# Kernel optimization log

Hardware: AMD Instinct MI355X
Metric: run time of the kernel (lower is better)

## Reference

```python
import jax, jax.numpy as jnp
import numpy as np
import math

B, S, D, H, FF, NB = 32, 512, 512, 8, 2048, 2
DK = D // H  # 64
NEG = -1e30  # stands in for torch's -1e32 (fp32-safe)


def _make_pe():
    # CosinePositionalEmbedding: deterministic sin/cos part (the 0.1*randn is fully overwritten)
    pos = np.arange(S, dtype=np.float32)[:, None]
    div = np.exp(np.arange(0, D, 2, dtype=np.float32) * -(math.log(10000.0) / D))
    pe = np.zeros((S, D), np.float32)
    pe[:, 0::2] = np.sin(pos * div)
    pe[:, 1::2] = np.cos(pos * div)
    return jnp.asarray(pe)[None]  # [1, S, D]


def setup_inputs() -> dict:
    key = jax.random.key(0)
    ks = jax.random.split(key, 10)
    def w(k, shape):
        return jax.random.normal(k, shape, jnp.float32) * 0.02
    return {
        "q_embed_data": jax.random.normal(ks[0], (B, S, D), jnp.float32),
        "qa_embed_data": jax.random.normal(ks[1], (B, S, D), jnp.float32),
        "forget_rate": jax.random.uniform(ks[2], (B, 1, S, 1), jnp.float32),
        "pe": _make_pe(),
        "Wk": w(ks[3], (NB, D, D)), "bk": jnp.zeros((NB, D), jnp.float32),
        "Wv": w(ks[4], (NB, D, D)), "bv": jnp.zeros((NB, D), jnp.float32),
        "Wo": w(ks[5], (NB, D, D)), "bo": jnp.zeros((NB, D), jnp.float32),
        "g1": jnp.ones((NB, D), jnp.float32), "be1": jnp.zeros((NB, D), jnp.float32),
        "W1": w(ks[6], (NB, D, FF)), "bf1": jnp.zeros((NB, FF), jnp.float32),
        "W2": w(ks[7], (NB, FF, D)), "bf2": jnp.zeros((NB, D), jnp.float32),
        "g2": jnp.ones((NB, D), jnp.float32), "be2": jnp.zeros((NB, D), jnp.float32),
    }


def _ln(x, g, b):
    m = jnp.mean(x, axis=-1, keepdims=True)
    v = jnp.var(x, axis=-1, keepdims=True)
    return (x - m) * jax.lax.rsqrt(v + 1e-5) * g + b


def reference(q_embed_data, qa_embed_data, forget_rate, pe, Wk, bk, Wv, bv, Wo, bo,
              g1, be1, W1, bf1, W2, bf2, g2, be2):
    x = q_embed_data + pe[:, :S]   # query stream
    y = qa_embed_data + pe[:, :S]  # value stream (constant across blocks)
    # mask==0 path: src_mask True where triu(k=0)==0, i.e. strictly-past positions j < i
    allowed = jnp.tril(jnp.ones((S, S), bool), k=-1)
    scale = 1.0 / math.sqrt(DK)
    for i in range(NB):
        # kq_same=True: q and k both use k_linear; query=key=x so q == k
        q = (x @ Wk[i] + bk[i]).reshape(B, S, H, DK).transpose(0, 2, 1, 3)  # [B,H,S,dk]
        k = q
        v = (y @ Wv[i] + bv[i]).reshape(B, S, H, DK).transpose(0, 2, 1, 3)
        scores = jnp.einsum('bhqd,bhkd->bhqk', q, k) * scale      # [B,H,S,S]
        scores = scores * forget_rate                              # broadcast [B,1,S,1]
        scores = jnp.where(allowed, scores, NEG)                   # masked_fill(mask==0, -1e32)
        attn = jax.nn.softmax(scores, axis=-1)
        attn = attn.at[:, :, 0, :].set(0.0)                        # zero_pad first query row
        out = jnp.einsum('bhqk,bhkd->bhqd', attn, v)
        out = out.transpose(0, 2, 1, 3).reshape(B, S, D) @ Wo[i] + bo[i]
        x = _ln(x + out, g1[i], be1[i])
        ffn = jax.nn.relu(x @ W1[i] + bf1[i]) @ W2[i] + bf2[i]
        x = _ln(x + ffn, g2[i], be2[i])
    return x
```

## Files before the change

### kernel.cpp

```cpp
#include <hip/hip_runtime.h>

#define B_ 32
#define S_ 512
#define D_ 512
#define H_ 8
#define DK_ 64
#define FF_ 2048

typedef float f32x4 __attribute__((ext_vector_type(4)));
typedef __bf16 bf16x8 __attribute__((ext_vector_type(8)));
typedef __bf16 bf16x4 __attribute__((ext_vector_type(4)));

__device__ __forceinline__ void gld_lds16(const void* gptr, void* lptr) {
    auto g = (__attribute__((address_space(1))) void*)(unsigned long long)gptr;
    auto l = (__attribute__((address_space(3))) void*)(unsigned)(unsigned long long)lptr;
    __builtin_amdgcn_global_load_lds(g, l, 16, 0, 0);
}

__global__ __launch_bounds__(256) void prep_kernel(
    const float* __restrict__ q, const float* __restrict__ qa,
    const float* __restrict__ pe, __bf16* __restrict__ xbf,
    __bf16* __restrict__ ybf)
{
    const int n4 = B_ * S_ * D_ / 4;
    for (int i = blockIdx.x * blockDim.x + threadIdx.x; i < n4;
         i += gridDim.x * blockDim.x) {
        float4 pv = ((const float4*)pe)[i & (S_ * D_ / 4 - 1)];
        float4 qv = ((const float4*)q)[i];
        float4 av = ((const float4*)qa)[i];
        bf16x4 xb = {(__bf16)(qv.x + pv.x), (__bf16)(qv.y + pv.y),
                     (__bf16)(qv.z + pv.z), (__bf16)(qv.w + pv.w)};
        ((bf16x4*)xbf)[i] = xb;
        bf16x4 yb = {(__bf16)(av.x + pv.x), (__bf16)(av.y + pv.y),
                     (__bf16)(av.z + pv.z), (__bf16)(av.w + pv.w)};
        ((bf16x4*)ybf)[i] = yb;
    }
}

__device__ __forceinline__ void ttile(
    const float* __restrict__ in, __bf16* __restrict__ out,
    int R, int C, int bx, int by, int t)
{
    __shared__ float tile[32][33];
    const int tc = bx * 32, tr = by * 32;
    const int lx = t & 31, ly = t >> 5;
    #pragma unroll
    for (int yy = ly; yy < 32; yy += 8)
        tile[yy][lx] = in[(long)(tr + yy) * C + tc + lx];
    __syncthreads();
    #pragma unroll
    for (int yy = ly; yy < 32; yy += 8)
        out[(long)(tc + yy) * R + tr + lx] = (__bf16)tile[lx][yy];
}

__global__ __launch_bounds__(256) void transpose_all(
    const float* __restrict__ Wk, const float* __restrict__ Wv,
    const float* __restrict__ Wo, const float* __restrict__ W1,
    const float* __restrict__ W2, __bf16* __restrict__ ok,
    __bf16* __restrict__ ov, __bf16* __restrict__ oo,
    __bf16* __restrict__ o1, __bf16* __restrict__ o2)
{
    const int id = blockIdx.x, t = threadIdx.x;
    if (id < 1536) {
        const int z = id >> 8, r = id & 255;
        const int sel = z >> 1, i = z & 1;
        const float* src = sel == 0 ? Wk : (sel == 1 ? Wv : Wo);
        __bf16* dst = sel == 0 ? ok : (sel == 1 ? ov : oo);
        ttile(src + (long)i * 262144, dst + (long)i * 262144, 512, 512,
              r & 15, r >> 4, t);
    } else if (id < 3584) {
        int r = id - 1536; const int i = r >> 10; r &= 1023;
        ttile(W1 + (long)i * 1048576, o1 + (long)i * 1048576, 512, 2048,
              r & 63, r >> 6, t);
    } else {
        int r = id - 3584; const int i = r >> 10; r &= 1023;
        ttile(W2 + (long)i * 1048576, o2 + (long)i * 1048576, 2048, 512,
              r & 15, r >> 4, t);
    }
}

template <int RELU, int MODE>
__global__ __launch_bounds__(256) void gemm_kernel(
    const __bf16* __restrict__ A, const __bf16* __restrict__ Bt,
    const float* __restrict__ bias, const __bf16* __restrict__ res,
    __bf16* __restrict__ out, int M, int N, int K)
{
    __shared__ __bf16 As[2][128 * 64];
    __shared__ __bf16 Bs[2][128 * 64];
    const int t = threadIdx.x;
    const int lane = t & 63;
    const int wv = t >> 6, wr = wv >> 1, wc = wv & 1;
    const int lr = lane & 15, lk = lane >> 4;

    const int nwg = gridDim.x * gridDim.y;
    const int lin = blockIdx.y * gridDim.x + blockIdx.x;
    const int swz = (lin & 7) * (nwg >> 3) + (lin >> 3);
    const int m0 = (swz / gridDim.x) * 128, n0 = (swz % gridDim.x) * 128;

    const int srow = t >> 3;
    const int sslot = (t & 7) ^ (srow & 7);
    const __bf16* gA = A + (long)(m0 + srow) * K + sslot * 8;
    const __bf16* gB = Bt + (long)(n0 + srow) * K + sslot * 8;
    const long rstep = (long)32 * K;

    auto STAGE = [&](int bsel, int k0) {
        char* ldsA = (char*)As[bsel] + t * 16;
        char* ldsB = (char*)Bs[bsel] + t * 16;
        #pragma unroll
        for (int u = 0; u < 4; ++u) {
            gld_lds16(gA + u * rstep + k0, ldsA + u * 4096);
            gld_lds16(gB + u * rstep + k0, ldsB + u * 4096);
        }
    };

    f32x4 acc[4][4] = {};
    auto COMPUTE = [&](int bsel) {
        #pragma unroll
        for (int kk = 0; kk < 2; ++kk) {
            bf16x8 af[4], bfr[4];
            #pragma unroll
            for (int i = 0; i < 4; ++i) {
                const int rr = wr * 64 + i * 16 + lr;
                af[i] = *(const bf16x8*)((const char*)As[bsel] +
                        (rr << 7) + (((kk * 4 + lk) ^ (rr & 7)) << 4));
            }
            #pragma unroll
            for (int j = 0; j < 4; ++j) {
                const int rr = wc * 64 + j * 16 + lr;
                bfr[j] = *(const bf16x8*)((const char*)Bs[bsel] +
                         (rr << 7) + (((kk * 4 + lk) ^ (rr & 7)) << 4));
            }
            #pragma unroll
            for (int i = 0; i < 4; ++i)
                #pragma unroll
                for (int j = 0; j < 4; ++j)
                    acc[i][j] = __builtin_amdgcn_mfma_f32_16x16x32_bf16(
                        af[i], bfr[j], acc[i][j], 0, 0, 0);
        }
    };

    const int NT = K >> 6;
    STAGE(0, 0);
    STAGE(1, 64);
    for (int kt = 0; kt < NT - 1; ++kt) {
        asm volatile("s_waitcnt vmcnt(8)" ::: "memory");
        __builtin_amdgcn_s_barrier();
        COMPUTE(kt & 1);
        __builtin_amdgcn_s_barrier();
        if (kt + 2 < NT) STAGE(kt & 1, (kt + 2) << 6);
    }
    asm volatile("s_waitcnt vmcnt(0)" ::: "memory");
    __builtin_amdgcn_s_barrier();
    COMPUTE((NT - 1) & 1);

    #pragma unroll
    for (int i = 0; i < 4; ++i) {
        #pragma unroll
        for (int j = 0; j < 4; ++j) {
            const int n = n0 + wc * 64 + j * 16 + lr;
            const float bv = bias[n];
            #pragma unroll
            for (int r = 0; r < 4; ++r) {
                const int m = m0 + wr * 64 + i * 16 + lk * 4 + r;
                const long off = (long)m * N + n;
                float v = acc[i][j][r] + bv;
                if (MODE == 1) v += (float)res[off];
                if (RELU) v = v > 0.f ? v : 0.f;
                out[off] = (__bf16)v;
            }
        }
    }
}

__global__ __launch_bounds__(256) void gemm_kv(
    const __bf16* __restrict__ xbf, const __bf16* __restrict__ ybf,
    const __bf16* __restrict__ wkt, const __bf16* __restrict__ wvt,
    const float* __restrict__ bk, const float* __restrict__ bv,
    __bf16* __restrict__ kout, __bf16* __restrict__ vtout)
{
    constexpr int N = 512, K = 512;
    __shared__ __bf16 As[2][128 * 64];
    __shared__ __bf16 Bs[2][128 * 64];
    const int t = threadIdx.x;
    const int lane = t & 63;
    const int wv = t >> 6, wr = wv >> 1, wc = wv & 1;
    const int lr = lane & 15, lk = lane >> 4;
    const int zv = blockIdx.z;

    const __bf16* A  = zv ? ybf : xbf;
    const __bf16* Bt = zv ? wvt : wkt;
    const float* bias = zv ? bv : bk;
    __bf16* out = zv ? vtout : kout;

    const int nwg = gridDim.x * gridDim.y;
    const int lin = blockIdx.y * gridDim.x + blockIdx.x;
    const int swz = (lin & 7) * (nwg >> 3) + (lin >> 3);
    const int m0 = (swz / gridDim.x) * 128, n0 = (swz % gridDim.x) * 128;

    const int srow = t >> 3;
    const int sslot = (t & 7) ^ (srow & 7);
    const __bf16* gA = A + (long)(m0 + srow) * K + sslot * 8;
    const __bf16* gB = Bt + (long)(n0 + srow) * K + sslot * 8;
    const long rstep = (long)32 * K;

    auto STAGE = [&](int bsel, int k0) {
        char* ldsA = (char*)As[bsel] + t * 16;
        char* ldsB = (char*)Bs[bsel] + t * 16;
        #pragma unroll
        for (int u = 0; u < 4; ++u) {
            gld_lds16(gA + u * rstep + k0, ldsA + u * 4096);
            gld_lds16(gB + u * rstep + k0, ldsB + u * 4096);
        }
    };

    f32x4 acc[4][4] = {};
    auto COMPUTE = [&](int bsel) {
        #pragma unroll
        for (int kk = 0; kk < 2; ++kk) {
            bf16x8 af[4], bfr[4];
            #pragma unroll
            for (int i = 0; i < 4; ++i) {
                const int rr = wr * 64 + i * 16 + lr;
                af[i] = *(const bf16x8*)((const char*)As[bsel] +
                        (rr << 7) + (((kk * 4 + lk) ^ (rr & 7)) << 4));
            }
            #pragma unroll
            for (int j = 0; j < 4; ++j) {
                const int rr = wc * 64 + j * 16 + lr;
                bfr[j] = *(const bf16x8*)((const char*)Bs[bsel] +
                         (rr << 7) + (((kk * 4 + lk) ^ (rr & 7)) << 4));
            }
            #pragma unroll
            for (int i = 0; i < 4; ++i)
                #pragma unroll
                for (int j = 0; j < 4; ++j)
                    acc[i][j] = __builtin_amdgcn_mfma_f32_16x16x32_bf16(
                        af[i], bfr[j], acc[i][j], 0, 0, 0);
        }
    };

    const int NT = K >> 6;
    STAGE(0, 0);
    STAGE(1, 64);
    for (int kt = 0; kt < NT - 1; ++kt) {
        asm volatile("s_waitcnt vmcnt(8)" ::: "memory");
        __builtin_amdgcn_s_barrier();
        COMPUTE(kt & 1);
        __builtin_amdgcn_s_barrier();
        if (kt + 2 < NT) STAGE(kt & 1, (kt + 2) << 6);
    }
    asm volatile("s_waitcnt vmcnt(0)" ::: "memory");
    __builtin_amdgcn_s_barrier();
    COMPUTE((NT - 1) & 1);

    #pragma unroll
    for (int i = 0; i < 4; ++i) {
        #pragma unroll
        for (int j = 0; j < 4; ++j) {
            const int n = n0 + wc * 64 + j * 16 + lr;
            const float bvl = bias[n];
            if (zv) {
                const int mb = m0 + wr * 64 + i * 16 + lk * 4;
                const int b = mb >> 9, s = mb & 511;
                bf16x4 ov = {(__bf16)(acc[i][j][0] + bvl),
                             (__bf16)(acc[i][j][1] + bvl),
                             (__bf16)(acc[i][j][2] + bvl),
                             (__bf16)(acc[i][j][3] + bvl)};
                *(bf16x4*)(out + (((long)(b * 8 + (n >> 6)) * 64 + (n & 63)) << 9) + s) = ov;
            } else {
                #pragma unroll
                for (int r = 0; r < 4; ++r) {
                    const int m = m0 + wr * 64 + i * 16 + lk * 4 + r;
                    out[(long)m * N + n] = (__bf16)(acc[i][j][r] + bvl);
                }
            }
        }
    }
}

__global__ __launch_bounds__(256) void attn_kernel(
    const __bf16* __restrict__ Q, const __bf16* __restrict__ Vt,
    const float* __restrict__ fr, __bf16* __restrict__ Out)
{
    __shared__ __bf16 Ks[2][64 * 64];
    __shared__ __bf16 Vs[2][64 * 64];
    __shared__ __bf16 Plds[4][16 * 64];
    const int t = threadIdx.x;
    const int lane = t & 63, wv = t >> 6;
    const int lr = lane & 15, lk = lane >> 4;
    const int qb = blockIdx.x, h = blockIdx.y, b = blockIdx.z;
    const int qT = qb * 64 + wv * 16;

    const __bf16* qp = Q + (long)(b * S_ + qT + lr) * D_ + h * DK_ + lk * 8;
    const bf16x8 qf0 = *(const bf16x8*)qp;
    const bf16x8 qf1 = *(const bf16x8*)(qp + 32);

    float frv[4], ls[4];
    #pragma unroll
    for (int r = 0; r < 4; ++r) {
        frv[r] = fr[b * S_ + qT + lk * 4 + r] * 0.125f;
        ls[r] = 0.f;
    }
    f32x4 o[4] = {};

    const int srow = t >> 3;
    const int sslot = (t & 7) ^ (srow & 7);
    const __bf16* kstage = Q + (long)(b * S_ + srow) * D_ + h * DK_ + sslot * 8;
    const __bf16* vstage = Vt + ((long)(b * H_ + h) * DK_ + srow) * S_ + sslot * 8;
    __bf16* pl = &Plds[wv][0];
    const int sw = (lr & 7);

    auto STAGE = [&](int bsel, int ks) {
        gld_lds16(kstage + (long)ks * D_, (char*)Ks[bsel] + t * 16);
        gld_lds16(kstage + (long)(ks + 32) * D_, (char*)Ks[bsel] + 4096 + t * 16);
        gld_lds16(vstage + ks, (char*)Vs[bsel] + t * 16);
        gld_lds16(vstage + ks + 32 * S_, (char*)Vs[bsel] + 4096 + t * 16);
    };

    auto COMPUTE = [&](int bsel, int ks) {
        f32x4 sc[4] = {};
        #pragma unroll
        for (int j = 0; j < 4; ++j) {
            const char* kb = (const char*)Ks[bsel] + ((j * 16 + lr) << 7);
            const bf16x8 kf0 = *(const bf16x8*)(kb + ((lk ^ sw) << 4));
            const bf16x8 kf1 = *(const bf16x8*)(kb + (((lk + 4) ^ sw) << 4));
            sc[j] = __builtin_amdgcn_mfma_f32_16x16x32_bf16(qf0, kf0, sc[j], 0, 0, 0);
            sc[j] = __builtin_amdgcn_mfma_f32_16x16x32_bf16(qf1, kf1, sc[j], 0, 0, 0);
        }
        #pragma unroll
        for (int j = 0; j < 4; ++j) {
            const int col = ks + j * 16 + lr;
            const int c8 = j * 2 + (lr >> 3), cb = lr & 7;
            #pragma unroll
            for (int r = 0; r < 4; ++r) {
                const int row = lk * 4 + r;
                const int sidx = row * 64 + ((c8 ^ (row & 7)) << 3) + cb;
                const float e = __expf(sc[j][r] * frv[r]);
                const float p = (col < qT + row) ? e : 0.f;
                ls[r] += p;
                pl[sidx] = (__bf16)p;
            }
        }
        bf16x8 pf[2];
        #pragma unroll
        for (int kk = 0; kk < 2; ++kk) {
            const int ridx = lr * 64 + (((kk * 4 + lk) ^ sw) << 3);
            pf[kk] = *(const bf16x8*)&pl[ridx];
        }
        #pragma unroll
        for (int dt = 0; dt < 4; ++dt) {
            const char* vb = (const char*)Vs[bsel] + ((dt * 16 + lr) << 7);
            #pragma unroll
            for (int kk = 0; kk < 2; ++kk) {
                const bf16x8 vf = *(const bf16x8*)(vb + (((kk * 4 + lk) ^ sw) << 4));
                o[dt] = __builtin_amdgcn_mfma_f32_16x16x32_bf16(pf[kk], vf, o[dt], 0, 0, 0);
            }
        }
    };

    const int nt = qb + 1;
    STAGE(0, 0);
    if (nt > 1) STAGE(1, 64);
    for (int tt = 0; tt < nt - 1; ++tt) {
        asm volatile("s_waitcnt vmcnt(4)" ::: "memory");
        __builtin_amdgcn_s_barrier();
        COMPUTE(tt & 1, tt * 64);
        __builtin_amdgcn_s_barrier();
        if (tt + 2 < nt) STAGE(tt & 1, (tt + 2) * 64);
    }
    asm volatile("s_waitcnt vmcnt(0)" ::: "memory");
    __builtin_amdgcn_s_barrier();
    COMPUTE((nt - 1) & 1, (nt - 1) * 64);

    #pragma unroll
    for (int r = 0; r < 4; ++r) {
        #pragma unroll
        for (int d = 1; d < 16; d <<= 1)
            ls[r] += __shfl_xor(ls[r], d);
        const float inv = ls[r] > 0.f ? 1.f / ls[r] : 0.f;
        #pragma unroll
        for (int dt = 0; dt < 4; ++dt)
            Out[(long)(b * S_ + qT + lk * 4 + r) * D_ + h * DK_ + dt * 16 + lr] =
                (__bf16)(o[dt][r] * inv);
    }
}

__global__ __launch_bounds__(256) void ln_kernel(
    const __bf16* __restrict__ pre, const float* __restrict__ g,
    const float* __restrict__ be, float* __restrict__ xout,
    __bf16* __restrict__ xbf, int wf32)
{
    const int lane = threadIdx.x & 63, wv = threadIdx.x >> 6;
    const long row = (long)blockIdx.x * 4 + wv;
    const bf16x8 v = *(const bf16x8*)(pre + row * D_ + lane * 8);
    float f[8];
    #pragma unroll
    for (int k = 0; k < 8; ++k) f[k] = (float)v[k];
    float s = 0.f, ss = 0.f;
    #pragma unroll
    for (int k = 0; k < 8; ++k) { s += f[k]; ss += f[k] * f[k]; }
    #pragma unroll
    for (int d = 1; d < 64; d <<= 1) {
        s  += __shfl_xor(s, d);
        ss += __shfl_xor(ss, d);
    }
    const float mean = s * (1.f / 512.f);
    const float rstd = rsqrtf(ss * (1.f / 512.f) - mean * mean + 1e-5f);
    const float4 ga = ((const float4*)(g + lane * 8))[0];
    const float4 gc = ((const float4*)(g + lane * 8))[1];
    const float4 ba = ((const float4*)(be + lane * 8))[0];
    const float4 bc = ((const float4*)(be + lane * 8))[1];
    float o[8];
    o[0] = (f[0] - mean) * rstd * ga.x + ba.x;
    o[1] = (f[1] - mean) * rstd * ga.y + ba.y;
    o[2] = (f[2] - mean) * rstd * ga.z + ba.z;
    o[3] = (f[3] - mean) * rstd * ga.w + ba.w;
    o[4] = (f[4] - mean) * rstd * gc.x + bc.x;
    o[5] = (f[5] - mean) * rstd * gc.y + bc.y;
    o[6] = (f[6] - mean) * rstd * gc.z + bc.z;
    o[7] = (f[7] - mean) * rstd * gc.w + bc.w;
    bf16x8 xb = {(__bf16)o[0], (__bf16)o[1], (__bf16)o[2], (__bf16)o[3],
                 (__bf16)o[4], (__bf16)o[5], (__bf16)o[6], (__bf16)o[7]};
    *(bf16x8*)(xbf + row * D_ + lane * 8) = xb;
    if (wf32) {
        float* xo = xout + row * D_ + lane * 8;
        ((float4*)xo)[0] = make_float4(o[0], o[1], o[2], o[3]);
        ((float4*)xo)[1] = make_float4(o[4], o[5], o[6], o[7]);
    }
}

extern "C" void kernel_launch(void* const* d_in, const int* in_sizes, int n_in,
                              void* d_out, int out_size, void* d_ws, size_t ws_size,
                              hipStream_t stream) {
    const float* q_embed = (const float*)d_in[0];
    const float* qa_embed = (const float*)d_in[1];
    const float* fr  = (const float*)d_in[2];
    const float* pe  = (const float*)d_in[3];
    const float* Wk  = (const float*)d_in[4];
    const float* bk  = (const float*)d_in[5];
    const float* Wv  = (const float*)d_in[6];
    const float* bv  = (const float*)d_in[7];
    const float* Wo  = (const float*)d_in[8];
    const float* bo  = (const float*)d_in[9];
    const float* g1  = (const float*)d_in[10];
    const float* be1 = (const float*)d_in[11];
    const float* W1  = (const float*)d_in[12];
    const float* bf1 = (const float*)d_in[13];
    const float* W2  = (const float*)d_in[14];
    const float* bf2 = (const float*)d_in[15];
    const float* g2  = (const float*)d_in[16];
    const float* be2 = (const float*)d_in[17];

    char* ws = (char*)d_ws;
    __bf16* xbf   = (__bf16*)(ws + 0);
    __bf16* ybf   = (__bf16*)(ws + 16777216);
    __bf16* pool  = (__bf16*)(ws + 33554432);
    __bf16* preln = (__bf16*)(ws + 100663296);
    __bf16* wts   = (__bf16*)(ws + 117440512);

    __bf16* kbuf  = pool;
    __bf16* vtbuf = pool + 8388608;
    __bf16* abuf  = pool + 2 * 8388608;
    __bf16* f1buf = pool;

    __bf16* wkt = wts;
    __bf16* wvt = wts + 524288;
    __bf16* wot = wts + 1048576;
    __bf16* w1t = wts + 1572864;
    __bf16* w2t = wts + 3670016;

    transpose_all<<<5632, 256, 0, stream>>>(Wk, Wv, Wo, W1, W2,
                                            wkt, wvt, wot, w1t, w2t);
    prep_kernel<<<2048, 256, 0, stream>>>(q_embed, qa_embed, pe, xbf, ybf);

    for (int i = 0; i < 2; ++i) {
        gemm_kv<<<dim3(4, 128, 2), 256, 0, stream>>>(
            xbf, ybf, wkt + i * 262144, wvt + i * 262144,
            bk + i * 512, bv + i * 512, kbuf, vtbuf);
        attn_kernel<<<dim3(8, 8, 32), 256, 0, stream>>>(kbuf, vtbuf, fr, abuf);
        gemm_kernel<0, 1><<<dim3(4, 128), 256, 0, stream>>>(
            abuf, wot + i * 262144, bo + i * 512, xbf, preln, 16384, 512, 512);
        ln_kernel<<<4096, 256, 0, stream>>>(preln, g1 + i * 512, be1 + i * 512,
                                            (float*)d_out, xbf, 0);
        gemm_kernel<1, 0><<<dim3(16, 128), 256, 0, stream>>>(
            xbf, w1t + i * 1048576, bf1 + i * 2048, nullptr, f1buf, 16384, 2048, 512);
        gemm_kernel<0, 1><<<dim3(4, 128), 256, 0, stream>>>(
            f1buf, w2t + i * 1048576, bf2 + i * 512, xbf, preln, 16384, 512, 2048);
        ln_kernel<<<4096, 256, 0, stream>>>(preln, g2 + i * 512, be2 + i * 512,
                                            (float*)d_out, xbf, i == 1 ? 1 : 0);
    }
}
```

Before: 438.0 us.

## Add 256x256-tile 8-wave GEMM with split-K-half pipelining for FFN1

Adds a new GEMM kernel using 512 threads (8 waves) and a 256x256 output tile with a 128KB double-buffered LDS, interleaving half-tile LDS reads, async global-to-LDS loads and MFMA with priority hints. It also swizzles the workgroup order for L2 locality. Only the FFN up-projection (16384x2048x512, ReLU) uses it. The larger tile raises arithmetic intensity and reduces operand reloads, at the cost of heavy LDS use (one block per CU) and high register pressure from the 128 accumulators per lane.

Measured after the change: 434.9 us. About the same (-0.7%).

```diff
diff --git a/kernel.cpp b/kernel.cpp
--- a/kernel.cpp
+++ b/kernel.cpp
@@ -162,6 +162,119 @@
             #pragma unroll
             for (int r = 0; r < 4; ++r) {
                 const int m = m0 + wr * 64 + i * 16 + lk * 4 + r;
+                const long off = (long)m * N + n;
+                float v = acc[i][j][r] + bv;
+                if (MODE == 1) v += (float)res[off];
+                if (RELU) v = v > 0.f ? v : 0.f;
+                out[off] = (__bf16)v;
+            }
+        }
+    }
+}
+
+template <int RELU, int MODE>
+__global__ __launch_bounds__(512, 2) void gemm8_kernel(
+    const __bf16* __restrict__ A, const __bf16* __restrict__ Bt,
+    const float* __restrict__ bias, const __bf16* __restrict__ res,
+    __bf16* __restrict__ out, int M, int N, int K)
+{
+    __shared__ __bf16 lds[65536];
+    const int t = threadIdx.x;
+    const int lane = t & 63, wv = t >> 6;
+    const int wr = wv >> 2, wc = wv & 3;
+    const int lr = lane & 15, lk = lane >> 4;
+
+    const int nwg = gridDim.x * gridDim.y;
+    const int lin = blockIdx.y * gridDim.x + blockIdx.x;
+    const int swz = (lin & 7) * (nwg >> 3) + (lin >> 3);
+    const int m0 = (swz / gridDim.x) * 256, n0 = (swz % gridDim.x) * 256;
+
+    const int srcrow = lane >> 2, srccol = (lane & 3) * 8;
+    auto STG = [&](int isB, int kt2, int kk2, int pb) {
+        const __bf16* src = isB ? Bt : A;
+        const int base = isB ? n0 : m0;
+        #pragma unroll
+        for (int u = 0; u < 2; ++u) {
+            const int sr = u * 8 + wv;
+            const long g = (long)(base + sr * 16 + srcrow) * K + kt2 * 64 + kk2 * 32 + srccol;
+            char* d = (char*)lds + pb * 65536 + isB * 32768 + ((sr * 2 + kk2) << 10) + lane * 16;
+            gld_lds16(src + g, d);
+        }
+    };
+
+    f32x4 acc[8][4] = {};
+    bf16x8 af[4], bfr[4];
+    auto RDA = [&](int p, int kk, int mh) {
+        #pragma unroll
+        for (int i = 0; i < 4; ++i) {
+            const int sr = wr * 8 + mh * 4 + i;
+            af[i] = *(const bf16x8*)((const char*)lds + p * 65536 +
+                    ((sr * 2 + kk) << 10) + lr * 64 + lk * 16);
+        }
+    };
+    auto RDB = [&](int p, int kk) {
+        #pragma unroll
+        for (int j = 0; j < 4; ++j) {
+            const int sr = wc * 4 + j;
+            bfr[j] = *(const bf16x8*)((const char*)lds + p * 65536 + 32768 +
+                     ((sr * 2 + kk) << 10) + lr * 64 + lk * 16);
+        }
+    };
+    auto MM = [&](int mh) {
+        __builtin_amdgcn_s_setprio(1);
+        #pragma unroll
+        for (int i = 0; i < 4; ++i)
+            #pragma unroll
+            for (int j = 0; j < 4; ++j)
+                acc[mh * 4 + i][j] = __builtin_amdgcn_mfma_f32_16x16x32_bf16(
+                    af[i], bfr[j], acc[mh * 4 + i][j], 0, 0, 0);
+        __builtin_amdgcn_s_setprio(0);
+    };
+
+    const int NT = K >> 6;
+    STG(0, 0, 0, 0); STG(1, 0, 0, 0); STG(0, 0, 1, 0); STG(1, 0, 1, 0);
+    STG(0, 1, 0, 1); STG(1, 1, 0, 1);
+
+    for (int kt = 0; kt < NT - 1; ++kt) {
+        const int p = kt & 1;
+        asm volatile("s_waitcnt vmcnt(8)" ::: "memory");
+        __builtin_amdgcn_s_barrier();
+        RDA(p, 0, 0); RDB(p, 0); STG(0, kt + 1, 1, p ^ 1);
+        MM(0);
+        __builtin_amdgcn_s_barrier();
+        RDA(p, 0, 1); STG(1, kt + 1, 1, p ^ 1);
+        MM(1);
+        asm volatile("s_waitcnt vmcnt(8)" ::: "memory");
+        __builtin_amdgcn_s_barrier();
+        RDA(p, 1, 0); RDB(p, 1); if (kt + 2 < NT) STG(0, kt + 2, 0, p);
+        MM(0);
+        __builtin_amdgcn_s_barrier();
+        RDA(p, 1, 1); if (kt + 2 < NT) STG(1, kt + 2, 0, p);
+        MM(1);
+    }
+    {
+        const int p = (NT - 1) & 1;
+        asm volatile("s_waitcnt vmcnt(4)" ::: "memory");
+        __builtin_amdgcn_s_barrier();
+        RDA(p, 0, 0); RDB(p, 0); MM(0);
+        __builtin_amdgcn_s_barrier();
+        RDA(p, 0, 1); MM(1);
+        asm volatile("s_waitcnt vmcnt(0)" ::: "memory");
+        __builtin_amdgcn_s_barrier();
+        RDA(p, 1, 0); RDB(p, 1); MM(0);
+        __builtin_amdgcn_s_barrier();
+        RDA(p, 1, 1); MM(1);
+    }
+
+    #pragma unroll
+    for (int i = 0; i < 8; ++i) {
+        #pragma unroll
+        for (int j = 0; j < 4; ++j) {
+            const int n = n0 + wc * 64 + j * 16 + lr;
+            const float bv = bias[n];
+            #pragma unroll
+            for (int r = 0; r < 4; ++r) {
+                const int m = m0 + wr * 128 + i * 16 + lk * 4 + r;
                 const long off = (long)m * N + n;
                 float v = acc[i][j][r] + bv;
                 if (MODE == 1) v += (float)res[off];
@@ -482,7 +595,7 @@
             abuf, wot + i * 262144, bo + i * 512, xbf, preln, 16384, 512, 512);
         ln_kernel<<<4096, 256, 0, stream>>>(preln, g1 + i * 512, be1 + i * 512,
                                             (float*)d_out, xbf, 0);
-        gemm_kernel<1, 0><<<dim3(16, 128), 256, 0, stream>>>(
+        gemm8_kernel<1, 0><<<dim3(8, 64), 512, 0, stream>>>(
             xbf, w1t + i * 1048576, bf1 + i * 2048, nullptr, f1buf, 16384, 2048, 512);
         gemm_kernel<0, 1><<<dim3(4, 128), 256, 0, stream>>>(
             f1buf, w2t + i * 1048576, bf2 + i * 512, xbf, preln, 16384, 512, 2048);
```
